# Optimization experiments

Measured on AMD Instinct MI355X. Metric: run time of the kernel, lower is better.

The kernel has to match this reference:

```python
import jax, jax.numpy as jnp
import numpy as np

N_ATOMS = 100000
N_EDGES = 200000  # paired: edge 2i and 2i+1 are reverses of each other
N_MOLS = 4096
D_V, D_E, D_H = 133, 14, 512
DEPTH = 3
BN_EPS = 1e-5


def setup_inputs() -> dict:
    key = jax.random.key(0)
    ks = jax.random.split(key, 10)
    V = jax.random.normal(ks[0], (N_ATOMS, D_V), dtype=jnp.float32)
    E = jax.random.normal(ks[1], (N_EDGES, D_E), dtype=jnp.float32)
    # paired directed edges: (src,dst) at 2i, (dst,src) at 2i+1 -> rev index is i^1
    half = N_EDGES // 2
    s = jax.random.randint(ks[2], (half,), 0, N_ATOMS, dtype=jnp.int32)
    d = jax.random.randint(ks[3], (half,), 0, N_ATOMS, dtype=jnp.int32)
    edge_src = jnp.stack([s, d], axis=1).reshape(-1)
    edge_dst = jnp.stack([d, s], axis=1).reshape(-1)
    batch = jnp.sort(jax.random.randint(ks[4], (N_ATOMS,), 0, N_MOLS, dtype=jnp.int32))
    sc = 0.02
    W_i = jax.random.normal(ks[5], (D_V + D_E, D_H), dtype=jnp.float32) * sc
    W_h = jax.random.normal(ks[6], (D_H, D_H), dtype=jnp.float32) * sc
    W_o = jax.random.normal(ks[7], (D_V + D_H, D_H), dtype=jnp.float32) * sc
    b_o = jnp.zeros((D_H,), dtype=jnp.float32)
    gamma = jnp.ones((D_H,), dtype=jnp.float32)
    beta = jnp.zeros((D_H,), dtype=jnp.float32)
    return {"V": V, "E": E, "edge_src": edge_src, "edge_dst": edge_dst,
            "batch": batch, "W_i": W_i, "W_h": W_h, "W_o": W_o, "b_o": b_o,
            "gamma": gamma, "beta": beta}


def reference(V, E, edge_src, edge_dst, batch, W_i, W_h, W_o, b_o, gamma, beta):
    n_atoms = V.shape[0]
    n_edges = E.shape[0]
    rev = jnp.arange(n_edges, dtype=jnp.int32) ^ 1  # reverse-bond index

    # --- BondMessagePassing (chemprop v2) ---
    # initialize: H_0 = W_i([V[src] ; E]), H = relu(H_0)
    H0 = jnp.concatenate([V[edge_src], E], axis=1) @ W_i  # [n_edges, d_h]
    H = jax.nn.relu(H0)
    for _ in range(DEPTH - 1):
        # message: sum of incoming edge states at dst node, gathered at src,
        # minus the reverse edge's own state
        M_node = jax.ops.segment_sum(H, edge_dst, num_segments=n_atoms)
        M = M_node[edge_src] - H[rev]
        # update: H = relu(H_0 + W_h(M)) (dropout = 0)
        H = jax.nn.relu(H0 + M @ W_h)
    # finalize: aggregate edges to nodes, H_v = relu(W_o([V ; M_v]))
    M_v = jax.ops.segment_sum(H, edge_dst, num_segments=n_atoms)
    H_v = jax.nn.relu(jnp.concatenate([V, M_v], axis=1) @ W_o + b_o)  # [n_atoms, d_h]

    # --- MeanAggregation over batch ids ---
    sums = jax.ops.segment_sum(H_v, batch, num_segments=N_MOLS)
    counts = jax.ops.segment_sum(jnp.ones((n_atoms,), H_v.dtype), batch, num_segments=N_MOLS)
    h_mol = sums / jnp.maximum(counts, 1.0)[:, None]  # [n_mols, d_h]

    # --- BatchNorm1d (training mode: batch statistics, biased variance) ---
    mu = h_mol.mean(axis=0)
    var = h_mol.var(axis=0)
    return (h_mol - mu) * jax.lax.rsqrt(var + BN_EPS) * gamma + beta
```

## Files before the change

kernel.cpp:

```cpp
#include <hip/hip_runtime.h>

typedef _Float16 f16;
typedef _Float16 half8 __attribute__((ext_vector_type(8)));
typedef _Float16 half4v __attribute__((ext_vector_type(4)));
typedef float f32x4 __attribute__((ext_vector_type(4)));

#define N_ATOMS 100000
#define N_EDGES 200000
#define N_MOLS  4096
#define D_V 133
#define D_E 14
#define D_H 512
#define KC  672
#define KSE 21
#define LDA 40

__global__ void wt_build_swz(const float* __restrict__ W1, int r1,
                             const float* __restrict__ W2, int r2,
                             f16* __restrict__ WtS) {
    int gid = blockIdx.x * blockDim.x + threadIdx.x;
    if (gid >= D_H * KC) return;
    int n = gid / KC;
    int k = gid - n * KC;
    float x = 0.f;
    if (k < r1) x = W1[k * D_H + n];
    else if (k < r1 + r2) x = W2[(k - r1) * D_H + n];
    const int dst = ((((n >> 4) * KSE + (k >> 5)) << 6) + (((k >> 3) & 3) << 4) + (n & 15)) * 8 + (k & 7);
    WtS[dst] = (f16)x;
}

__global__ void csr_hist(const int* __restrict__ edst, int* __restrict__ cnt) {
    int e = blockIdx.x * blockDim.x + threadIdx.x;
    if (e < N_EDGES) atomicAdd(&cnt[edst[e]], 1);
}

__global__ __launch_bounds__(1024) void csr_scan(const int* __restrict__ cnt,
                                                 int* __restrict__ off, int* __restrict__ pos) {
    __shared__ int sums[1024];
    const int tid = threadIdx.x;
    const int lo = tid * 100;
    int s = 0;
    if (lo < N_ATOMS) {
        const int4* c4 = reinterpret_cast<const int4*>(cnt + lo);
        #pragma unroll
        for (int i = 0; i < 25; ++i) { int4 v = c4[i]; s += v.x + v.y + v.z + v.w; }
    }
    sums[tid] = s;
    __syncthreads();
    for (int d = 1; d < 1024; d <<= 1) {
        int v = (tid >= d) ? sums[tid - d] : 0;
        __syncthreads();
        sums[tid] += v;
        __syncthreads();
    }
    int run = sums[tid] - s;
    if (lo < N_ATOMS) {
        const int4* c4 = reinterpret_cast<const int4*>(cnt + lo);
        for (int i = 0; i < 25; ++i) {
            int4 v = c4[i];
            const int b = lo + i * 4;
            off[b]     = run; pos[b]     = run; run += v.x;
            off[b + 1] = run; pos[b + 1] = run; run += v.y;
            off[b + 2] = run; pos[b + 2] = run; run += v.z;
            off[b + 3] = run; pos[b + 3] = run; run += v.w;
        }
    }
    if (tid == 1023) off[N_ATOMS] = run;
}

__global__ void csr_scatter(const int* __restrict__ edst, int* __restrict__ pos,
                            int* __restrict__ eid) {
    int e = blockIdx.x * blockDim.x + threadIdx.x;
    if (e < N_EDGES) {
        int idx = atomicAdd(&pos[edst[e]], 1);
        eid[idx] = e;
    }
}

template<bool F16M>
__global__ __launch_bounds__(512) void seg_csr(
    const f16* __restrict__ H, const int* __restrict__ off, const int* __restrict__ eid,
    void* __restrict__ MnOut, float* __restrict__ Msc)
{
    const int n = blockIdx.x * 8 + (threadIdx.x >> 6);
    const int lane = threadIdx.x & 63;
    const int j0 = off[n], j1 = off[n + 1];
    float acc[8];
    #pragma unroll
    for (int k = 0; k < 8; ++k) acc[k] = 0.f;
    int e_cur = (j0 < j1) ? eid[j0] : 0;
    for (int j = j0; j < j1; ++j) {
        const int e_nxt = (j + 1 < j1) ? eid[j + 1] : 0;
        const half8 h = *reinterpret_cast<const half8*>(&H[e_cur * D_H + lane * 8]);
        #pragma unroll
        for (int k = 0; k < 8; ++k) acc[k] += (float)h[k];
        e_cur = e_nxt;
    }
    if (F16M) {
        half8 o;
        #pragma unroll
        for (int k = 0; k < 8; ++k) o[k] = (f16)acc[k];
        *reinterpret_cast<half8*>(&((f16*)MnOut)[n * D_H + lane * 8]) = o;
    } else {
        float m = 0.f;
        #pragma unroll
        for (int k = 0; k < 8; ++k) m = fmaxf(m, fabsf(acc[k]));
        m = fmaxf(m, __shfl_xor(m, 1));
        m = fmaxf(m, __shfl_xor(m, 2));
        m = fmaxf(m, 1e-20f);
        const float s = m * (1.f / 127.f);
        const float inv_s = 127.f / m;
        if ((lane & 3) == 0) Msc[n * 16 + (lane >> 2)] = s;
        int q[8];
        #pragma unroll
        for (int k = 0; k < 8; ++k) q[k] = __float2int_rn(acc[k] * inv_s);
        uint2 o;
        o.x = (q[0] & 0xff) | ((q[1] & 0xff) << 8) | ((q[2] & 0xff) << 16) | ((unsigned)(q[3] & 0xff) << 24);
        o.y = (q[4] & 0xff) | ((q[5] & 0xff) << 8) | ((q[6] & 0xff) << 16) | ((unsigned)(q[7] & 0xff) << 24);
        *reinterpret_cast<uint2*>(&((unsigned int*)MnOut)[n * 128 + lane * 2]) = o;
    }
}

template<bool F16M, int KS0>
__global__ __launch_bounds__(512, 4) void gemm_pass(
    const float* __restrict__ V, const float* __restrict__ E,
    const int* __restrict__ esrc, const void* __restrict__ Mn,
    const float* __restrict__ Msc,
    f16* __restrict__ Ha, const f16* __restrict__ WtS)
{
    __shared__ __align__(16) f16 Al[2][64 * LDA];
    const int tid = threadIdx.x;
    const int rowblk = blockIdx.x << 6;
    const int srow = tid >> 3;
    const int skk  = (tid & 7) << 2;
    const int e_s  = rowblk + srow;
    const int sv   = esrc[e_s];
    const int rev  = e_s ^ 1;
    const int lane = tid & 63;
    const int quad = lane >> 4;
    const int m16  = lane & 15;
    const int colbase = (tid >> 6) << 6;
    const int cb0 = (tid >> 6) << 2;
    const f16* WtL = WtS + lane * 8;

    f32x4 acc[4][4];
    #pragma unroll
    for (int a = 0; a < 4; ++a)
    #pragma unroll
    for (int b = 0; b < 4; ++b)
    #pragma unroll
    for (int r = 0; r < 4; ++r) acc[a][b][r] = 0.f;

    char4 pq0, pq1, pq2; float ps0, ps1, ps2;
    half4v pm0, pm1, pm2; half4v ph0, ph1, ph2;
    float pv0[4], pv1[4], pv2[4];

#define GP_ISSUE(S, KSV) do {                                                        \
    const int ks_i_ = (KSV);                                                         \
    if (ks_i_ < KSE) {                                                               \
        const int k0_ = ks_i_ << 5;                                                  \
        if (k0_ < D_H) {                                                             \
            if (F16M) {                                                              \
                pm##S = *reinterpret_cast<const half4v*>(&((const f16*)Mn)[sv * D_H + k0_ + skk]); \
            } else {                                                                 \
                pq##S = *reinterpret_cast<const char4*>(&((const char*)Mn)[sv * D_H + k0_ + skk]); \
                ps##S = Msc[sv * 16 + (k0_ >> 5)];                                   \
            }                                                                        \
            ph##S = *reinterpret_cast<const half4v*>(&Ha[rev * D_H + k0_ + skk]);    \
        } else {                                                                     \
            const int kb_ = k0_ + skk - D_H;                                         \
            pv##S[0] = (kb_ + 0 < D_V) ? V[sv * D_V + kb_ + 0] : ((kb_ + 0 < D_V + D_E) ? E[e_s * D_E + kb_ + 0 - D_V] : 0.f); \
            pv##S[1] = (kb_ + 1 < D_V) ? V[sv * D_V + kb_ + 1] : ((kb_ + 1 < D_V + D_E) ? E[e_s * D_E + kb_ + 1 - D_V] : 0.f); \
            pv##S[2] = (kb_ + 2 < D_V) ? V[sv * D_V + kb_ + 2] : ((kb_ + 2 < D_V + D_E) ? E[e_s * D_E + kb_ + 2 - D_V] : 0.f); \
            pv##S[3] = (kb_ + 3 < D_V) ? V[sv * D_V + kb_ + 3] : ((kb_ + 3 < D_V + D_E) ? E[e_s * D_E + kb_ + 3 - D_V] : 0.f); \
        }                                                                            \
    }                                                                                \
} while (0)

#define GP_MAKEW(S, KSV, W) do {                                                     \
    const int k0_ = (KSV) << 5;                                                      \
    if (k0_ < D_H) {                                                                 \
        if (F16M) { W = pm##S - ph##S; }                                             \
        else {                                                                       \
            W[0] = (f16)((float)pq##S.x * ps##S - (float)ph##S[0]);                  \
            W[1] = (f16)((float)pq##S.y * ps##S - (float)ph##S[1]);                  \
            W[2] = (f16)((float)pq##S.z * ps##S - (float)ph##S[2]);                  \
            W[3] = (f16)((float)pq##S.w * ps##S - (float)ph##S[3]);                  \
        }                                                                            \
    } else {                                                                         \
        W[0] = (f16)pv##S[0]; W[1] = (f16)pv##S[1];                                  \
        W[2] = (f16)pv##S[2]; W[3] = (f16)pv##S[3];                                  \
    }                                                                                \
} while (0)

    GP_ISSUE(0, KS0);
    GP_ISSUE(1, KS0 + 1);
    GP_ISSUE(2, KS0 + 2);
    {
        half4v w;
        GP_MAKEW(0, KS0, w);
        *reinterpret_cast<half4v*>(&Al[0][srow * LDA + skk]) = w;
        GP_ISSUE(0, KS0 + 3);
    }
    __syncthreads();

    #pragma unroll
    for (int ks = KS0; ks < KSE; ++ks) {
        const int i = ks - KS0;
        const int cur = i & 1;
        if (ks + 1 < KSE) {
            const int sl = (i + 1) % 3;
            half4v w;
            if (sl == 0)      GP_MAKEW(0, ks + 1, w);
            else if (sl == 1) GP_MAKEW(1, ks + 1, w);
            else              GP_MAKEW(2, ks + 1, w);
            *reinterpret_cast<half4v*>(&Al[cur ^ 1][srow * LDA + skk]) = w;
            if (sl == 0)      GP_ISSUE(0, ks + 4);
            else if (sl == 1) GP_ISSUE(1, ks + 4);
            else              GP_ISSUE(2, ks + 4);
        }
        half8 af[4];
        #pragma unroll
        for (int rt = 0; rt < 4; ++rt)
            af[rt] = *reinterpret_cast<const half8*>(&Al[cur][(rt * 16 + m16) * LDA + quad * 8]);
        #pragma unroll
        for (int ct = 0; ct < 4; ++ct) {
            const half8 bf = *reinterpret_cast<const half8*>(&WtL[(((cb0 + ct) * KSE + ks) << 9)]);
            #pragma unroll
            for (int rt = 0; rt < 4; ++rt)
                acc[rt][ct] = __builtin_amdgcn_mfma_f32_16x16x32_f16(af[rt], bf, acc[rt][ct], 0, 0, 0);
        }
        __syncthreads();
    }
#undef GP_ISSUE
#undef GP_MAKEW

    #pragma unroll
    for (int rt = 0; rt < 4; ++rt)
    #pragma unroll
    for (int ct = 0; ct < 4; ++ct)
    #pragma unroll
    for (int r = 0; r < 4; ++r) {
        const int row = rowblk + rt * 16 + quad * 4 + r;
        const int col = colbase + ct * 16 + m16;
        Ha[row * D_H + col] = (f16)fmaxf(acc[rt][ct][r], 0.f);
    }
}

template<bool F16M>
__global__ __launch_bounds__(512, 4) void gemm_out(
    const float* __restrict__ V, const void* __restrict__ Mn,
    const float* __restrict__ Msc, const float* __restrict__ bo,
    const f16* __restrict__ WtS, f16* __restrict__ Hv)
{
    __shared__ __align__(16) f16 Al[2][64 * LDA];
    __shared__ float bo_s[D_H];
    const int tid = threadIdx.x;
    const int rowblk = blockIdx.x << 6;
    bo_s[tid] = bo[tid];
    const int srow = tid >> 3;
    const int skk  = (tid & 7) << 2;
    const int arow = min(rowblk + srow, N_ATOMS - 1);
    const int lane = tid & 63;
    const int quad = lane >> 4;
    const int m16  = lane & 15;
    const int colbase = (tid >> 6) << 6;
    const int cb0 = (tid >> 6) << 2;
    const f16* WtL = WtS + lane * 8;

    f32x4 acc[4][4];
    #pragma unroll
    for (int a = 0; a < 4; ++a)
    #pragma unroll
    for (int b = 0; b < 4; ++b)
    #pragma unroll
    for (int r = 0; r < 4; ++r) acc[a][b][r] = 0.f;

    char4 pq0, pq1, pq2; float ps0, ps1, ps2;
    half4v pm0, pm1, pm2;
    float pv0[4], pv1[4], pv2[4];

#define GO_ISSUE(S, KSV) do {                                                        \
    const int ks_i_ = (KSV);                                                         \
    if (ks_i_ < KSE) {                                                               \
        const int k0_ = ks_i_ << 5;                                                  \
        if (k0_ < D_H) {                                                             \
            if (F16M) {                                                              \
                pm##S = *reinterpret_cast<const half4v*>(&((const f16*)Mn)[arow * D_H + k0_ + skk]); \
            } else {                                                                 \
                pq##S = *reinterpret_cast<const char4*>(&((const char*)Mn)[arow * D_H + k0_ + skk]); \
                ps##S = Msc[arow * 16 + (k0_ >> 5)];                                 \
            }                                                                        \
        } else {                                                                     \
            const int kb_ = k0_ + skk - D_H;                                         \
            pv##S[0] = (kb_ + 0 < D_V) ? V[arow * D_V + kb_ + 0] : 0.f;              \
            pv##S[1] = (kb_ + 1 < D_V) ? V[arow * D_V + kb_ + 1] : 0.f;              \
            pv##S[2] = (kb_ + 2 < D_V) ? V[arow * D_V + kb_ + 2] : 0.f;              \
            pv##S[3] = (kb_ + 3 < D_V) ? V[arow * D_V + kb_ + 3] : 0.f;              \
        }                                                                            \
    }                                                                                \
} while (0)

#define GO_MAKEW(S, KSV, W) do {                                                     \
    const int k0_ = (KSV) << 5;                                                      \
    if (k0_ < D_H) {                                                                 \
        if (F16M) { W = pm##S; }                                                     \
        else {                                                                       \
            W[0] = (f16)((float)pq##S.x * ps##S);                                    \
            W[1] = (f16)((float)pq##S.y * ps##S);                                    \
            W[2] = (f16)((float)pq##S.z * ps##S);                                    \
            W[3] = (f16)((float)pq##S.w * ps##S);                                    \
        }                                                                            \
    } else {                                                                         \
        W[0] = (f16)pv##S[0]; W[1] = (f16)pv##S[1];                                  \
        W[2] = (f16)pv##S[2]; W[3] = (f16)pv##S[3];                                  \
    }                                                                                \
} while (0)

    GO_ISSUE(0, 0);
    GO_ISSUE(1, 1);
    GO_ISSUE(2, 2);
    {
        half4v w;
        GO_MAKEW(0, 0, w);
        *reinterpret_cast<half4v*>(&Al[0][srow * LDA + skk]) = w;
        GO_ISSUE(0, 3);
    }
    __syncthreads();

    #pragma unroll
    for (int ks = 0; ks < KSE; ++ks) {
        const int cur = ks & 1;
        if (ks + 1 < KSE) {
            const int sl = (ks + 1) % 3;
            half4v w;
            if (sl == 0)      GO_MAKEW(0, ks + 1, w);
            else if (sl == 1) GO_MAKEW(1, ks + 1, w);
            else              GO_MAKEW(2, ks + 1, w);
            *reinterpret_cast<half4v*>(&Al[cur ^ 1][srow * LDA + skk]) = w;
            if (sl == 0)      GO_ISSUE(0, ks + 4);
            else if (sl == 1) GO_ISSUE(1, ks + 4);
            else              GO_ISSUE(2, ks + 4);
        }
        half8 af[4];
        #pragma unroll
        for (int rt = 0; rt < 4; ++rt)
            af[rt] = *reinterpret_cast<const half8*>(&Al[cur][(rt * 16 + m16) * LDA + quad * 8]);
        #pragma unroll
        for (int ct = 0; ct < 4; ++ct) {
            const half8 bf = *reinterpret_cast<const half8*>(&WtL[(((cb0 + ct) * KSE + ks) << 9)]);
            #pragma unroll
            for (int rt = 0; rt < 4; ++rt)
                acc[rt][ct] = __builtin_amdgcn_mfma_f32_16x16x32_f16(af[rt], bf, acc[rt][ct], 0, 0, 0);
        }
        __syncthreads();
    }
#undef GO_ISSUE
#undef GO_MAKEW

    #pragma unroll
    for (int rt = 0; rt < 4; ++rt)
    #pragma unroll
    for (int ct = 0; ct < 4; ++ct)
    #pragma unroll
    for (int r = 0; r < 4; ++r) {
        const int row = rowblk + rt * 16 + quad * 4 + r;
        if (row < N_ATOMS) {
            const int col = colbase + ct * 16 + m16;
            Hv[row * D_H + col] = (f16)fmaxf(acc[rt][ct][r] + bo_s[col], 0.f);
        }
    }
}

__global__ __launch_bounds__(512) void mol_mean(
    const f16* __restrict__ Hv, const int* __restrict__ batch, float* __restrict__ mean)
{
    const int m = blockIdx.x;
    __shared__ int sh[2];
    if (threadIdx.x == 0) {
        int lo = 0, hi = N_ATOMS;
        while (lo < hi) { int mid = (lo + hi) >> 1; if (batch[mid] < m) lo = mid + 1; else hi = mid; }
        sh[0] = lo;
        int lo2 = lo; hi = N_ATOMS;
        while (lo2 < hi) { int mid = (lo2 + hi) >> 1; if (batch[mid] < m + 1) lo2 = mid + 1; else hi = mid; }
        sh[1] = lo2;
    }
    __syncthreads();
    const int a0 = sh[0], a1 = sh[1];
    float acc = 0.f;
    for (int a = a0; a < a1; ++a) acc += (float)Hv[(size_t)a * D_H + threadIdx.x];
    mean[m * D_H + threadIdx.x] = acc / (float)max(a1 - a0, 1);
}

__global__ __launch_bounds__(256) void bn_stats(
    const float* __restrict__ mean_in, const float* __restrict__ gamma,
    const float* __restrict__ beta, float* __restrict__ An, float* __restrict__ Bn)
{
    const int n = blockIdx.x;
    const int tid = threadIdx.x;
    float s = 0.f, s2 = 0.f;
    for (int m = tid; m < N_MOLS; m += 256) {
        float h = mean_in[m * D_H + n];
        s += h; s2 += h * h;
    }
    for (int off = 32; off > 0; off >>= 1) {
        s  += __shfl_down(s, off);
        s2 += __shfl_down(s2, off);
    }
    __shared__ float sh[8];
    const int wave = tid >> 6, lane = tid & 63;
    if (lane == 0) { sh[wave] = s; sh[4 + wave] = s2; }
    __syncthreads();
    if (tid == 0) {
        float S  = sh[0] + sh[1] + sh[2] + sh[3];
        float S2 = sh[4] + sh[5] + sh[6] + sh[7];
        float mu = S / (float)N_MOLS;
        float var = fmaxf(S2 / (float)N_MOLS - mu * mu, 0.f);
        float sc = rsqrtf(var + 1e-5f) * gamma[n];
        An[n] = sc;
        Bn[n] = beta[n] - mu * sc;
    }
}

__global__ void bn_apply(const float* __restrict__ mean_in,
                         const float* __restrict__ An, const float* __restrict__ Bn,
                         float* __restrict__ out)
{
    int gid = blockIdx.x * blockDim.x + threadIdx.x;
    int n = gid & 511;
    out[gid] = mean_in[gid] * An[n] + Bn[n];
}

extern "C" void kernel_launch(void* const* d_in, const int* in_sizes, int n_in,
                              void* d_out, int out_size, void* d_ws, size_t ws_size,
                              hipStream_t stream)
{
    (void)in_sizes; (void)n_in; (void)out_size;
    const float* V     = (const float*)d_in[0];
    const float* E     = (const float*)d_in[1];
    const int*   esrc  = (const int*)d_in[2];
    const int*   edst  = (const int*)d_in[3];
    const int*   batch = (const int*)d_in[4];
    const float* Wi    = (const float*)d_in[5];
    const float* Wh    = (const float*)d_in[6];
    const float* Wo    = (const float*)d_in[7];
    const float* bo    = (const float*)d_in[8];
    const float* gam   = (const float*)d_in[9];
    const float* bet   = (const float*)d_in[10];
    float* out = (float*)d_out;

    char* ws = (char*)d_ws;
    f16*   WtC  = (f16*)(ws + 0);
    f16*   WtO  = (f16*)(ws + 688128);
    int*   off  = (int*)(ws + 1376256);
    int*   eid  = (int*)(ws + 1776384);
    int*   cnt  = (int*)(ws + 2576384);
    float* An   = (float*)(ws + 2992768);
    float* Bn   = (float*)(ws + 2994816);
    f16*   Ha   = (f16*)(ws + 2996864);
    void*  Mn   = (void*)(ws + 207796864);
    float* Msc  = (float*)(ws + 258996864);
    f16*   Hv   = Ha;
    float* mean = out;

    const bool f16m = ws_size >= 310196864ULL;

    wt_build_swz<<<(D_H * KC + 255) / 256, 256, 0, stream>>>(Wh, D_H, Wi, D_V + D_E, WtC);
    wt_build_swz<<<(D_H * KC + 255) / 256, 256, 0, stream>>>(Wo + D_V * D_H, D_H, Wo, D_V, WtO);

    hipMemsetAsync(cnt, 0, 400000, stream);
    csr_hist<<<(N_EDGES + 511) / 512, 512, 0, stream>>>(edst, cnt);
    csr_scan<<<1, 1024, 0, stream>>>(cnt, off, cnt);
    csr_scatter<<<(N_EDGES + 511) / 512, 512, 0, stream>>>(edst, cnt, eid);

    if (f16m) {
        gemm_pass<true, 16><<<N_EDGES / 64, 512, 0, stream>>>(V, E, esrc, Mn, Msc, Ha, WtC);
        for (int it = 0; it < 2; ++it) {
            seg_csr<true><<<N_ATOMS / 8, 512, 0, stream>>>(Ha, off, eid, Mn, Msc);
            gemm_pass<true, 0><<<N_EDGES / 64, 512, 0, stream>>>(V, E, esrc, Mn, Msc, Ha, WtC);
        }
        seg_csr<true><<<N_ATOMS / 8, 512, 0, stream>>>(Ha, off, eid, Mn, Msc);
        gemm_out<true><<<(N_ATOMS + 63) / 64, 512, 0, stream>>>(V, Mn, Msc, bo, WtO, Hv);
    } else {
        gemm_pass<false, 16><<<N_EDGES / 64, 512, 0, stream>>>(V, E, esrc, Mn, Msc, Ha, WtC);
        for (int it = 0; it < 2; ++it) {
            seg_csr<false><<<N_ATOMS / 8, 512, 0, stream>>>(Ha, off, eid, Mn, Msc);
            gemm_pass<false, 0><<<N_EDGES / 64, 512, 0, stream>>>(V, E, esrc, Mn, Msc, Ha, WtC);
        }
        seg_csr<false><<<N_ATOMS / 8, 512, 0, stream>>>(Ha, off, eid, Mn, Msc);
        gemm_out<false><<<(N_ATOMS + 63) / 64, 512, 0, stream>>>(V, Mn, Msc, bo, WtO, Hv);
    }

    mol_mean<<<N_MOLS, 512, 0, stream>>>(Hv, batch, mean);
    bn_stats<<<D_H, 256, 0, stream>>>(mean, gam, bet, An, Bn);
    bn_apply<<<(N_MOLS * D_H) / 256, 256, 0, stream>>>(mean, An, Bn, out);
}
```

Measured before the change: 1.440 ms.

## Shrink prefetch pipeline to two stages and drop launch-bounds occupancy hint

Reduces the register prefetch ring in both GEMM kernels from three slots (lookahead of 3 k-steps) to two slots (lookahead of 2). The fully unrolled k-loop becomes an unroll-by-2 loop with a peeled final MFMA step, which removes the in-loop tail branch. The minimum-blocks-per-SM hint is removed from the launch bounds. Together these cut code size and register pressure and give the compiler freedom over register allocation, at the cost of less global-load latency hiding and possibly lower occupancy.

```diff
diff --git a/kernel.cpp b/kernel.cpp
--- a/kernel.cpp
+++ b/kernel.cpp
@@ -122,7 +122,7 @@
 }
 
 template<bool F16M, int KS0>
-__global__ __launch_bounds__(512, 4) void gemm_pass(
+__global__ __launch_bounds__(512) void gemm_pass(
     const float* __restrict__ V, const float* __restrict__ E,
     const int* __restrict__ esrc, const void* __restrict__ Mn,
     const float* __restrict__ Msc,
@@ -151,9 +151,9 @@
     #pragma unroll
     for (int r = 0; r < 4; ++r) acc[a][b][r] = 0.f;
 
-    char4 pq0, pq1, pq2; float ps0, ps1, ps2;
-    half4v pm0, pm1, pm2; half4v ph0, ph1, ph2;
-    float pv0[4], pv1[4], pv2[4];
+    char4 pq0, pq1; float ps0, ps1;
+    half4v pm0, pm1; half4v ph0, ph1;
+    float pv0[4], pv1[4];
 
 #define GP_ISSUE(S, KSV) do {                                                        \
     const int ks_i_ = (KSV);                                                         \
@@ -193,47 +193,51 @@
     }                                                                                \
 } while (0)
 
+#define GP_MFMA(KSV, CUR) do {                                                       \
+    half8 af[4];                                                                     \
+    _Pragma("unroll")                                                                \
+    for (int rt = 0; rt < 4; ++rt)                                                   \
+        af[rt] = *reinterpret_cast<const half8*>(&Al[CUR][(rt * 16 + m16) * LDA + quad * 8]); \
+    _Pragma("unroll")                                                                \
+    for (int ct = 0; ct < 4; ++ct) {                                                 \
+        const half8 bf = *reinterpret_cast<const half8*>(&WtL[(((cb0 + ct) * KSE + (KSV)) << 9)]); \
+        _Pragma("unroll")                                                            \
+        for (int rt = 0; rt < 4; ++rt)                                               \
+            acc[rt][ct] = __builtin_amdgcn_mfma_f32_16x16x32_f16(af[rt], bf, acc[rt][ct], 0, 0, 0); \
+    }                                                                                \
+} while (0)
+
     GP_ISSUE(0, KS0);
     GP_ISSUE(1, KS0 + 1);
-    GP_ISSUE(2, KS0 + 2);
     {
         half4v w;
         GP_MAKEW(0, KS0, w);
         *reinterpret_cast<half4v*>(&Al[0][srow * LDA + skk]) = w;
-        GP_ISSUE(0, KS0 + 3);
+        GP_ISSUE(0, KS0 + 2);
     }
     __syncthreads();
 
-    #pragma unroll
-    for (int ks = KS0; ks < KSE; ++ks) {
-        const int i = ks - KS0;
+    constexpr int NT = KSE - KS0;
+    #pragma unroll 2
+    for (int i = 0; i < NT - 1; ++i) {
+        const int ks = KS0 + i;
         const int cur = i & 1;
-        if (ks + 1 < KSE) {
-            const int sl = (i + 1) % 3;
+        {
             half4v w;
-            if (sl == 0)      GP_MAKEW(0, ks + 1, w);
-            else if (sl == 1) GP_MAKEW(1, ks + 1, w);
-            else              GP_MAKEW(2, ks + 1, w);
+            if ((i + 1) & 1) { GP_MAKEW(1, ks + 1, w); }
+            else             { GP_MAKEW(0, ks + 1, w); }
             *reinterpret_cast<half4v*>(&Al[cur ^ 1][srow * LDA + skk]) = w;
-            if (sl == 0)      GP_ISSUE(0, ks + 4);
-            else if (sl == 1) GP_ISSUE(1, ks + 4);
-            else              GP_ISSUE(2, ks + 4);
+            if ((i + 1) & 1) { GP_ISSUE(1, ks + 3); }
+            else             { GP_ISSUE(0, ks + 3); }
         }
-        half8 af[4];
-        #pragma unroll
-        for (int rt = 0; rt < 4; ++rt)
-            af[rt] = *reinterpret_cast<const half8*>(&Al[cur][(rt * 16 + m16) * LDA + quad * 8]);
-        #pragma unroll
-        for (int ct = 0; ct < 4; ++ct) {
-            const half8 bf = *reinterpret_cast<const half8*>(&WtL[(((cb0 + ct) * KSE + ks) << 9)]);
-            #pragma unroll
-            for (int rt = 0; rt < 4; ++rt)
-                acc[rt][ct] = __builtin_amdgcn_mfma_f32_16x16x32_f16(af[rt], bf, acc[rt][ct], 0, 0, 0);
-        }
+        GP_MFMA(ks, cur);
         __syncthreads();
     }
+    GP_MFMA(KSE - 1, (NT - 1) & 1);
+
 #undef GP_ISSUE
 #undef GP_MAKEW
+#undef GP_MFMA
 
     #pragma unroll
     for (int rt = 0; rt < 4; ++rt)
@@ -248,7 +252,7 @@
 }
 
 template<bool F16M>
-__global__ __launch_bounds__(512, 4) void gemm_out(
+__global__ __launch_bounds__(512) void gemm_out(
     const float* __restrict__ V, const void* __restrict__ Mn,
     const float* __restrict__ Msc, const float* __restrict__ bo,
     const f16* __restrict__ WtS, f16* __restrict__ Hv)
@@ -276,9 +280,9 @@
     #pragma unroll
     for (int r = 0; r < 4; ++r) acc[a][b][r] = 0.f;
 
-    char4 pq0, pq1, pq2; float ps0, ps1, ps2;
-    half4v pm0, pm1, pm2;
-    float pv0[4], pv1[4], pv2[4];
+    char4 pq0, pq1; float ps0, ps1;
+    half4v pm0, pm1;
+    float pv0[4], pv1[4];
 
 #define GO_ISSUE(S, KSV) do {                                                        \
     const int ks_i_ = (KSV);                                                         \
@@ -317,46 +321,50 @@
     }                                                                                \
 } while (0)
 
+#define GO_MFMA(KSV, CUR) do {                                                       \
+    half8 af[4];                                                                     \
+    _Pragma("unroll")                                                                \
+    for (int rt = 0; rt < 4; ++rt)                                                   \
+        af[rt] = *reinterpret_cast<const half8*>(&Al[CUR][(rt * 16 + m16) * LDA + quad * 8]); \
+    _Pragma("unroll")                                                                \
+    for (int ct = 0; ct < 4; ++ct) {                                                 \
+        const half8 bf = *reinterpret_cast<const half8*>(&WtL[(((cb0 + ct) * KSE + (KSV)) << 9)]); \
+        _Pragma("unroll")                                                            \
+        for (int rt = 0; rt < 4; ++rt)                                               \
+            acc[rt][ct] = __builtin_amdgcn_mfma_f32_16x16x32_f16(af[rt], bf, acc[rt][ct], 0, 0, 0); \
+    }                                                                                \
+} while (0)
+
     GO_ISSUE(0, 0);
     GO_ISSUE(1, 1);
-    GO_ISSUE(2, 2);
     {
         half4v w;
         GO_MAKEW(0, 0, w);
         *reinterpret_cast<half4v*>(&Al[0][srow * LDA + skk]) = w;
-        GO_ISSUE(0, 3);
+        GO_ISSUE(0, 2);
     }
     __syncthreads();
 
-    #pragma unroll
-    for (int ks = 0; ks < KSE; ++ks) {
-        const int cur = ks & 1;
-        if (ks + 1 < KSE) {
-            const int sl = (ks + 1) % 3;
+    #pragma unroll 2
+    for (int i = 0; i < KSE - 1; ++i) {
+        const int ks = i;
+        const int cur = i & 1;
+        {
             half4v w;
-            if (sl == 0)      GO_MAKEW(0, ks + 1, w);
-            else if (sl == 1) GO_MAKEW(1, ks + 1, w);
-            else              GO_MAKEW(2, ks + 1, w);
+            if ((i + 1) & 1) { GO_MAKEW(1, ks + 1, w); }
+            else             { GO_MAKEW(0, ks + 1, w); }
             *reinterpret_cast<half4v*>(&Al[cur ^ 1][srow * LDA + skk]) = w;
-            if (sl == 0)      GO_ISSUE(0, ks + 4);
-            else if (sl == 1) GO_ISSUE(1, ks + 4);
-            else              GO_ISSUE(2, ks + 4);
+            if ((i + 1) & 1) { GO_ISSUE(1, ks + 3); }
+            else             { GO_ISSUE(0, ks + 3); }
         }
-        half8 af[4];
-        #pragma unroll
-        for (int rt = 0; rt < 4; ++rt)
-            af[rt] = *reinterpret_cast<const half8*>(&Al[cur][(rt * 16 + m16) * LDA + quad * 8]);
-        #pragma unroll
-        for (int ct = 0; ct < 4; ++ct) {
-            const half8 bf = *reinterpret_cast<const half8*>(&WtL[(((cb0 + ct) * KSE + ks) << 9)]);
-            #pragma unroll
-            for (int rt = 0; rt < 4; ++rt)
-                acc[rt][ct] = __builtin_amdgcn_mfma_f32_16x16x32_f16(af[rt], bf, acc[rt][ct], 0, 0, 0);
-        }
+        GO_MFMA(ks, cur);
         __syncthreads();
     }
+    GO_MFMA(KSE - 1, (KSE - 1) & 1);
+
 #undef GO_ISSUE
 #undef GO_MAKEW
+#undef GO_MFMA
 
     #pragma unroll
     for (int rt = 0; rt < 4; ++rt)
```

New measurement: 1.512 ms. 5.0% more time.
